# Kernel tuning notes

Hardware: AMD Instinct MI355X
Metric: run time of the kernel (lower is better)

The kernel has to match this reference:

```python
import jax, jax.numpy as jnp
import numpy as np

LAMBDA_COORD = 5.0
LAMBDA_NOOBJ = 0.5
B, N, F = 2048, 64, 19  # batch, nb_pred, 2 + n_classes


def _greedy_scan(Permut, v, h, D2, mask, n):
    # One greedy-assignment phase: n sequential argmax/one-hot steps.
    def step(carry, _):
        Permut, v, h, D2 = carry
        D2 = D2 * v[:, :, None] * h[:, None, :]
        A = jax.nn.one_hot(jnp.argmax(D2, axis=-1), n, dtype=D2.dtype)          # row-wise best col
        Bm = v[:, :, None] * A * D2
        C = jnp.swapaxes(jax.nn.one_hot(jnp.argmax(Bm, axis=-2), n, dtype=D2.dtype), -1, -2)  # col-wise best row
        E = v[:, :, None] * A * C
        Permut = Permut + E
        v = (1.0 - Permut.sum(-1)) * mask
        h = 1.0 - Permut.sum(-2)
        return (Permut, v, h, D2), None
    (Permut, v, h, D2), _ = jax.lax.scan(step, (Permut, v, h, D2), None, length=n)
    return Permut, v, h, D2


def _permute_ypred(y_true, y_pred):
    alpha = y_true[:, :, 0]                      # [B, N] in {0,1}
    x = y_true[:, :, 1]
    p = y_pred[:, :, 1]
    n = x.shape[-1]
    D1 = 1.0 - jnp.abs(x[:, :, None] - p[:, None, :])   # [B, N, N] similarity

    # Phase 1: match ground-truth positives (rows with alpha=1).
    Permut0 = jnp.zeros_like(D1)
    v0 = alpha
    h0 = jnp.ones_like(alpha)
    D2_0 = v0[:, :, None] * D1
    Permut, v, h, _ = _greedy_scan(Permut0, v0, h0, D2_0, alpha, n)

    # Phase 2: match remaining rows (alpha=0) to remaining predictions.
    neg = 1.0 - alpha
    D2_1 = neg[:, :, None] * D1 * h[:, None, :]
    Permut, _, _, _ = _greedy_scan(Permut, neg, h, D2_1, neg, n)

    permutation = jnp.argmax(Permut, axis=-1)            # [B, N]
    idx = jnp.broadcast_to(permutation[:, :, None], y_pred.shape)
    return jnp.take_along_axis(y_pred, idx, axis=1)


def setup_inputs() -> dict:
    key = jax.random.key(0)
    k1, k2, k3 = jax.random.split(key, 3)
    y_true = jax.random.uniform(k1, (B, N, F), dtype=jnp.float32)
    alpha = (jax.random.uniform(k3, (B, N)) < 0.3).astype(jnp.float32)
    y_true = y_true.at[:, :, 0].set(alpha)
    y_pred = jax.random.uniform(k2, (B, N, F), dtype=jnp.float32)
    return {"y_true": y_true, "y_pred": y_pred}


def reference(y_true, y_pred):
    y_pred = _permute_ypred(y_true, y_pred)
    a = y_true[:, :, 0]
    loss = jnp.sum(
        a * LAMBDA_COORD * jnp.square(y_true[:, :, 1] - y_pred[:, :, 1])
        + a * jnp.square(a - y_pred[:, :, 0])
        + (1.0 - a) * LAMBDA_NOOBJ * jnp.square(a - y_pred[:, :, 0])
        + a * jnp.sum(jnp.square(y_true[:, :, 2:] - y_pred[:, :, 2:]), axis=-1)
    )
    return loss
```

## Files before the change

kernel.cpp:

```cpp
#include <hip/hip_runtime.h>
#include <stdint.h>


#define NN 64
#define NF 19

__global__ __launch_bounds__(64) void spotting_loss_kernel(
    const float* __restrict__ yt, const float* __restrict__ yp,
    float* __restrict__ out)
{
  const int b = blockIdx.x;
  const int i = threadIdx.x;
  const float* __restrict__ ytb = yt + (size_t)b * NN * NF;
  const float* __restrict__ ypb = yp + (size_t)b * NN * NF;

  __shared__ float p_sh[NN];
  __shared__ unsigned long long key_sh[NN];

  const float alpha = ytb[i * NF + 0];
  const float x     = ytb[i * NF + 1];
  p_sh[i] = ypb[i * NF + 1];
  __syncthreads();

  float D1r[NN];
#pragma unroll
  for (int j = 0; j < NN; ++j) {
    D1r[j] = 1.0f - fabsf(x - p_sh[j]);
  }

  unsigned long long hbits = ~0ull;
  int   perm  = 0;
  int   jmax  = 0;
  float best  = 0.0f;

  for (int phase = 0; phase < 2; ++phase) {
    bool vlive  = (phase == 0) ? (alpha > 0.5f) : (alpha < 0.5f);
    bool rescan = vlive;

    for (int it = 0; it < NN; ++it) {
      if (__ballot(vlive) == 0ull) break;

      if (rescan) {
        const unsigned hlo = (unsigned)hbits;
        const unsigned hhi = (unsigned)(hbits >> 32);
        best = -1.0f; jmax = 0;
#pragma unroll
        for (int j = 0; j < NN; ++j) {
          const unsigned bit = (j < 32) ? ((hlo >> j) & 1u)
                                        : ((hhi >> (j - 32)) & 1u);
          const unsigned msk = 0u - bit;
          const float t = __uint_as_float(__float_as_uint(D1r[j]) & msk);
          if (t > best) { best = t; jmax = j; }
        }
        rescan = false;
      }

      key_sh[i] = 63ull;
      __syncthreads();

      if (vlive && best > 0.0f) {
        const unsigned long long key =
            (((unsigned long long)__float_as_uint(best)) << 6) |
            (unsigned long long)(63 - i);
        atomicMax(&key_sh[jmax], key);
      }
      __syncthreads();

      const unsigned long long kc = key_sh[i];
      const bool colkill = (kc >> 6) != 0ull;
      const unsigned long long killed = __ballot(colkill);

      if (vlive) {
        const unsigned long long kw = key_sh[jmax];
        const int winner = 63 - (int)(kw & 63ull);
        if (winner == i) {
          perm = jmax;
          vlive = false;
        } else if ((killed >> jmax) & 1ull) {
          rescan = true;
        }
      }
      hbits &= ~killed;
      __syncthreads();
    }
  }

  const float* __restrict__ ypr = ypb + (size_t)perm * NF;
  const float a  = alpha;
  const float p0 = ypr[0];
  const float p1 = ypr[1];
  const float dx = x - p1;
  const float da = a - p0;
  float s2 = 0.0f;
#pragma unroll
  for (int f = 2; f < NF; ++f) {
    const float d = ytb[i * NF + f] - ypr[f];
    s2 += d * d;
  }
  float l = a * 5.0f * (dx * dx)
          + a * (da * da)
          + (1.0f - a) * 0.5f * (da * da)
          + a * s2;

#pragma unroll
  for (int off = 32; off > 0; off >>= 1) l += __shfl_down(l, off);
  if (i == 0) atomicAdd(out, l);
}

extern "C" void kernel_launch(void* const* d_in, const int* in_sizes, int n_in,
                              void* d_out, int out_size, void* d_ws, size_t ws_size,
                              hipStream_t stream) {
  const float* yt = (const float*)d_in[0];
  const float* yp = (const float*)d_in[1];
  float* out = (float*)d_out;
  const int B = in_sizes[0] / (NN * NF);

  hipMemsetAsync(out, 0, sizeof(float) * (size_t)out_size, stream);
  spotting_loss_kernel<<<B, 64, 0, stream>>>(yt, yp, out);
}
```

Before: 106.5 us.

## Stage inputs in LDS with float4 loads and tag keys to drop block barriers

Copies each batch row of y_true and y_pred into shared memory with coalesced float4 loads, so the final loss gather reads LDS rather than strided global memory. Replaces the per-iteration reset of the atomic key array with an iteration tag in the high bits of the key, which removes one barrier per step. The remaining __syncthreads are swapped for wave barriers because the block is a single 64-lane wavefront. This relies on wave64 execution and on LDS atomics being visible after a wave barrier, and the larger LDS footprint may lower occupancy.

```diff
diff --git a/kernel.cpp b/kernel.cpp
--- a/kernel.cpp
+++ b/kernel.cpp
@@ -4,6 +4,8 @@
 
 #define NN 64
 #define NF 19
+#define ROWF (NN * NF)
+#define ROW4 (ROWF / 4)
 
 __global__ __launch_bounds__(64) void spotting_loss_kernel(
     const float* __restrict__ yt, const float* __restrict__ yp,
@@ -11,27 +13,47 @@
 {
   const int b = blockIdx.x;
   const int i = threadIdx.x;
-  const float* __restrict__ ytb = yt + (size_t)b * NN * NF;
-  const float* __restrict__ ypb = yp + (size_t)b * NN * NF;
 
+  __shared__ float yt_sh[ROWF];
+  __shared__ float yp_sh[ROWF];
   __shared__ float p_sh[NN];
   __shared__ unsigned long long key_sh[NN];
 
-  const float alpha = ytb[i * NF + 0];
-  const float x     = ytb[i * NF + 1];
-  p_sh[i] = ypb[i * NF + 1];
+  const float4* __restrict__ yt4 = (const float4*)(yt + (size_t)b * ROWF);
+  const float4* __restrict__ yp4 = (const float4*)(yp + (size_t)b * ROWF);
+  float4* yt_sh4 = (float4*)yt_sh;
+  float4* yp_sh4 = (float4*)yp_sh;
+#pragma unroll
+  for (int t = 0; t < 5; ++t) {
+    const int idx = t * NN + i;
+    if (idx < ROW4) {
+      yt_sh4[idx] = yt4[idx];
+      yp_sh4[idx] = yp4[idx];
+    }
+  }
+  key_sh[i] = 0ull;
+  __syncthreads();
+
+  const float alpha = yt_sh[i * NF + 0];
+  const float x     = yt_sh[i * NF + 1];
+  p_sh[i] = yp_sh[i * NF + 1];
   __syncthreads();
 
   float D1r[NN];
+  const float4* __restrict__ p4 = (const float4*)p_sh;
 #pragma unroll
-  for (int j = 0; j < NN; ++j) {
-    D1r[j] = 1.0f - fabsf(x - p_sh[j]);
+  for (int j4 = 0; j4 < NN / 4; ++j4) {
+    const float4 pv = p4[j4];
+    D1r[4 * j4 + 0] = 1.0f - fabsf(x - pv.x);
+    D1r[4 * j4 + 1] = 1.0f - fabsf(x - pv.y);
+    D1r[4 * j4 + 2] = 1.0f - fabsf(x - pv.z);
+    D1r[4 * j4 + 3] = 1.0f - fabsf(x - pv.w);
   }
 
   unsigned long long hbits = ~0ull;
-  int   perm  = 0;
-  int   jmax  = 0;
-  float best  = 0.0f;
+  int perm = 0, jmax = 0;
+  float best = 0.0f;
+  unsigned tag = 0;
 
   for (int phase = 0; phase < 2; ++phase) {
     bool vlive  = (phase == 0) ? (alpha > 0.5f) : (alpha < 0.5f);
@@ -39,6 +61,7 @@
 
     for (int it = 0; it < NN; ++it) {
       if (__ballot(vlive) == 0ull) break;
+      ++tag;
 
       if (rescan) {
         const unsigned hlo = (unsigned)hbits;
@@ -48,32 +71,28 @@
         for (int j = 0; j < NN; ++j) {
           const unsigned bit = (j < 32) ? ((hlo >> j) & 1u)
                                         : ((hhi >> (j - 32)) & 1u);
-          const unsigned msk = 0u - bit;
-          const float t = __uint_as_float(__float_as_uint(D1r[j]) & msk);
+          const float t = __uint_as_float(__float_as_uint(D1r[j]) & (0u - bit));
           if (t > best) { best = t; jmax = j; }
         }
         rescan = false;
       }
 
-      key_sh[i] = 63ull;
-      __syncthreads();
-
       if (vlive && best > 0.0f) {
         const unsigned long long key =
-            (((unsigned long long)__float_as_uint(best)) << 6) |
+            ((unsigned long long)tag << 38) |
+            ((unsigned long long)__float_as_uint(best) << 6) |
             (unsigned long long)(63 - i);
         atomicMax(&key_sh[jmax], key);
       }
-      __syncthreads();
+      __builtin_amdgcn_wave_barrier();
 
       const unsigned long long kc = key_sh[i];
-      const bool colkill = (kc >> 6) != 0ull;
-      const unsigned long long killed = __ballot(colkill);
+      const unsigned long long killed =
+          __ballot((unsigned)(kc >> 38) == tag);
 
-      if (vlive) {
+      if (vlive && best > 0.0f) {
         const unsigned long long kw = key_sh[jmax];
-        const int winner = 63 - (int)(kw & 63ull);
-        if (winner == i) {
+        if ((int)(63ull - (kw & 63ull)) == i) {
           perm = jmax;
           vlive = false;
         } else if ((killed >> jmax) & 1ull) {
@@ -81,20 +100,20 @@
         }
       }
       hbits &= ~killed;
-      __syncthreads();
+      __builtin_amdgcn_wave_barrier();
     }
   }
 
-  const float* __restrict__ ypr = ypb + (size_t)perm * NF;
-  const float a  = alpha;
-  const float p0 = ypr[0];
-  const float p1 = ypr[1];
+  const float a = alpha;
+  const int pbase = perm * NF;
+  const float p0 = yp_sh[pbase + 0];
+  const float p1 = yp_sh[pbase + 1];
   const float dx = x - p1;
   const float da = a - p0;
   float s2 = 0.0f;
 #pragma unroll
   for (int f = 2; f < NF; ++f) {
-    const float d = ytb[i * NF + f] - ypr[f];
+    const float d = yt_sh[i * NF + f] - yp_sh[pbase + f];
     s2 += d * d;
   }
   float l = a * 5.0f * (dx * dx)
@@ -113,7 +132,7 @@
   const float* yt = (const float*)d_in[0];
   const float* yp = (const float*)d_in[1];
   float* out = (float*)d_out;
-  const int B = in_sizes[0] / (NN * NF);
+  const int B = in_sizes[0] / ROWF;
 
   hipMemsetAsync(out, 0, sizeof(float) * (size_t)out_size, stream);
   spotting_loss_kernel<<<B, 64, 0, stream>>>(yt, yp, out);
```

Result: slower. 108.9 us (+2.3%).
